# Kernel tuning notes

Hardware: AMD Instinct MI355X
Metric: run time of the kernel (lower is better)

The kernel has to match this reference:

```python
import jax, jax.numpy as jnp
import numpy as np

EPS = 1e-5
GN_GROUPS = 4  # ConvBlock groupnorm num_groups

def _conv3d(x, w, b):
    # x: [B,C,D,H,W], w: [O,I,3,3,3]
    y = jax.lax.conv_general_dilated(x, w, (1, 1, 1), 'SAME',
                                     dimension_numbers=('NCDHW', 'OIDHW', 'NCDHW'))
    return y + b[None, :, None, None, None]

def _groupnorm(x, gamma, beta):
    b, c, d, h, w = x.shape
    xg = x.reshape(b, GN_GROUPS, c // GN_GROUPS, d, h, w)
    m = xg.mean(axis=(2, 3, 4, 5), keepdims=True)
    v = xg.var(axis=(2, 3, 4, 5), keepdims=True)
    xn = ((xg - m) * jax.lax.rsqrt(v + EPS)).reshape(b, c, d, h, w)
    return xn * gamma[None, :, None, None, None] + beta[None, :, None, None, None]

def setup_inputs() -> dict:
    key = jax.random.key(0)
    ks = jax.random.split(key, 8)
    B, C, D, H, W = 4, 64, 16, 16, 16
    R = 4
    f = lambda k, s: jax.random.normal(k, s, dtype=jnp.float32) * 0.05
    return {
        'x': jax.random.normal(ks[0], (B, C, D, H, W), dtype=jnp.float32),
        'w_i': f(ks[1], (C, C, 3, 3, 3)), 'b_i': jnp.zeros((C,), jnp.float32),
        'gamma_i': jnp.ones((C,), jnp.float32), 'beta_i': jnp.zeros((C,), jnp.float32),
        'w_q': f(ks[2], (C // R, C)), 'b_q': jnp.zeros((C // R,), jnp.float32),
        'w_k': f(ks[3], (C // R, C)), 'b_k': jnp.zeros((C // R,), jnp.float32),
        'w_v': f(ks[4], (C, C)), 'b_v': jnp.zeros((C,), jnp.float32),
        'w_o': f(ks[5], (C, C, 3, 3, 3)), 'b_o': jnp.zeros((C,), jnp.float32),
        'gamma_o': jnp.ones((C,), jnp.float32), 'beta_o': jnp.zeros((C,), jnp.float32),
    }

def reference(x, w_i, b_i, gamma_i, beta_i, w_q, b_q, w_k, b_k, w_v, b_v,
              w_o, b_o, gamma_o, beta_o):
    # i_conv: Conv3d(3x3x3) -> GroupNorm(4) -> ReLU
    x = jax.nn.relu(_groupnorm(_conv3d(x, w_i, b_i), gamma_i, beta_i))
    b, c, d, h, w = x.shape
    n = d * h * w
    xf = x.reshape(b, c, n)
    # spatial attention (groups=1): conv1x1 projections as channel matmuls
    q = jnp.einsum('oc,bcn->bon', w_q, xf) + b_q[None, :, None]   # [b, c/r, n]
    k = jnp.einsum('oc,bcn->bon', w_k, xf) + b_k[None, :, None]   # [b, c/r, n]
    v = jnp.einsum('oc,bcn->bon', w_v, xf) + b_v[None, :, None]   # [b, c,   n]
    A = jax.nn.softmax(jnp.einsum('bqn,bqm->bnm', q, k), axis=-1)  # [b, n, n]
    # ans = bmm(value, A^T): ans[b,c,m] = sum_n v[b,c,n] * A[b,m,n]
    sa = jnp.einsum('bcn,bmn->bcm', v, A).reshape(b, c, d, h, w)
    # channel attention
    Ac = jax.nn.softmax(jnp.einsum('bcn,bdn->bcd', xf, xf), axis=-1)  # [b, c, c]
    ca = jnp.einsum('bcd,bdn->bcn', Ac, xf).reshape(b, c, d, h, w)
    y = x + sa + ca
    # o_conv
    return jax.nn.relu(_groupnorm(_conv3d(y, w_o, b_o), gamma_o, beta_o))
```

## Files before the change

### kernel.cpp

```cpp
#include <hip/hip_runtime.h>

#define OFF_T0  0
#define OFF_SA  1048576
#define OFF_QT  2097152
#define OFF_KT  2359296
#define OFF_VB  2621440
#define OFF_YT  3145728
#define OFF_XB  3670016
#define OFF_AC  4194304
#define OFF_WBI 4210688
#define OFF_WBO 4265984
#define OFF_PT  4321280
#define OFF_PO  4325376
#define OFF_MS  6422528
#define WS_NEED ((size_t)6553600 * 4)

typedef __attribute__((ext_vector_type(8))) short short8v;
typedef __attribute__((ext_vector_type(4))) short short4v;
typedef __attribute__((ext_vector_type(4))) float f32x4;

__device__ __forceinline__ ushort f2bf(float f) {
  union { float f; unsigned u; } v; v.f = f;
  unsigned r = (v.u + 0x7fffu + ((v.u >> 16) & 1u)) >> 16;
  return (ushort)r;
}
__device__ __forceinline__ float bf2f(ushort u) {
  union { unsigned u; float f; } v; v.u = ((unsigned)u) << 16;
  return v.f;
}

__global__ __launch_bounds__(256) void wcvt2_k(const float* __restrict__ wi, const float* __restrict__ wo,
    ushort* __restrict__ wbi, ushort* __restrict__ wbo) {
  int idx = blockIdx.x * 256 + threadIdx.x;
  const float* w = idx < 110592 ? wi : wo;
  ushort* wb = idx < 110592 ? wbi : wbo;
  int j = idx < 110592 ? idx : idx - 110592;
  int ci = j & 63, tap = (j >> 6) % 27, co = j / (64 * 27);
  wb[j] = f2bf(w[(co * 64 + ci) * 27 + tap]);
}

__global__ __launch_bounds__(256) void xcvt_k(const float* __restrict__ x, ushort* __restrict__ xb,
    float* __restrict__ pt) {
  if (blockIdx.x == 0 && threadIdx.x < 64) pt[threadIdx.x] = 0.f;
  __shared__ ushort tl[64 * 72];
  int b = blockIdx.x >> 6;
  int n0 = (blockIdx.x & 63) * 64;
  int t = threadIdx.x;
  int ci = t >> 2, q = t & 3;
  const float* src = x + (size_t)(b * 64 + ci) * 4096 + n0 + q * 16;
  #pragma unroll
  for (int i = 0; i < 4; ++i) {
    float4 v = *reinterpret_cast<const float4*>(src + i * 4);
    tl[(q * 16 + i * 4 + 0) * 72 + ci] = f2bf(v.x);
    tl[(q * 16 + i * 4 + 1) * 72 + ci] = f2bf(v.y);
    tl[(q * 16 + i * 4 + 2) * 72 + ci] = f2bf(v.z);
    tl[(q * 16 + i * 4 + 3) * 72 + ci] = f2bf(v.w);
  }
  __syncthreads();
  int n = t >> 2, qq = t & 3;
  ushort* dst = xb + (size_t)(b * 4096 + n0 + n) * 64 + qq * 16;
  *reinterpret_cast<short8v*>(dst) = *reinterpret_cast<const short8v*>(&tl[n * 72 + qq * 16]);
  *reinterpret_cast<short8v*>(dst + 8) = *reinterpret_cast<const short8v*>(&tl[n * 72 + qq * 16 + 8]);
}

__global__ __launch_bounds__(256) void conv_mfma_k(const ushort* __restrict__ xt,
    const ushort* __restrict__ wb, const float* __restrict__ bias, float* __restrict__ out,
    float* __restrict__ ptg) {
  __shared__ __align__(16) ushort xls[18 * 18 * 64];
  __shared__ float sh_st[16];
  int blk = blockIdx.x;
  int h0 = (blk & 3) * 4;
  int d0 = (blk >> 2) & 15;
  int b  = blk >> 6;
  int tid = threadIdx.x;

  const ushort* xtb = xt + (size_t)b * 4096 * 64;
  for (int u = tid; u < 324; u += 256) {
    int w_s = u % 18;
    int row = u / 18;
    int dz = row / 6, h_s = row - dz * 6;
    int d = d0 + dz - 1, h = h0 + h_s - 1, w = w_s - 1;
    ushort* dst = &xls[(row * 18 + w_s) * 64];
    int swz = w_s & 7;
    if (d >= 0 && d < 16 && h >= 0 && h < 16 && w >= 0 && w < 16) {
      const ushort* src = xtb + (size_t)(d * 256 + h * 16 + w) * 64;
      #pragma unroll
      for (int c = 0; c < 8; ++c)
        *reinterpret_cast<short8v*>(dst + ((c ^ swz) << 3)) =
            *reinterpret_cast<const short8v*>(src + (c << 3));
    } else {
      short8v z = {};
      #pragma unroll
      for (int c = 0; c < 8; ++c)
        *reinterpret_cast<short8v*>(dst + ((c ^ swz) << 3)) = z;
    }
  }
  __syncthreads();

  int wv = tid >> 6, l = tid & 63;
  int wn = wv >> 1, wc = wv & 1;
  int lm = l & 15, lg = l >> 4;

  f32x4 acc[2][2] = {};
  const ushort* wbase0 = wb + (size_t)((wc * 2 + 0) * 16 + lm) * 1728 + lg * 8;
  const ushort* wbase1 = wb + (size_t)((wc * 2 + 1) * 16 + lm) * 1728 + lg * 8;

  #pragma unroll 6
  for (int s = 0; s < 54; ++s) {
    int tap = s >> 1, c0h = s & 1;
    int dz = tap / 9, dyx = tap - dz * 9;
    int dy = dyx / 3, dx = dyx - dy * 3;
    int wrow = lm + dx;
    int chunk = ((c0h * 4 + lg) ^ (wrow & 7)) << 3;
    int r0 = ((dz * 6 + wn * 2 + dy) * 18 + wrow) * 64 + chunk;
    short8v a0 = *reinterpret_cast<const short8v*>(&xls[r0]);
    short8v a1 = *reinterpret_cast<const short8v*>(&xls[r0 + 18 * 64]);
    short8v b0 = *reinterpret_cast<const short8v*>(wbase0 + s * 32);
    short8v b1 = *reinterpret_cast<const short8v*>(wbase1 + s * 32);
    acc[0][0] = __builtin_amdgcn_mfma_f32_16x16x32_bf16(a0, b0, acc[0][0], 0, 0, 0);
    acc[0][1] = __builtin_amdgcn_mfma_f32_16x16x32_bf16(a0, b1, acc[0][1], 0, 0, 0);
    acc[1][0] = __builtin_amdgcn_mfma_f32_16x16x32_bf16(a1, b0, acc[1][0], 0, 0, 0);
    acc[1][1] = __builtin_amdgcn_mfma_f32_16x16x32_bf16(a1, b1, acc[1][1], 0, 0, 0);
  }

  float gs[2], gss[2];
  #pragma unroll
  for (int j = 0; j < 2; ++j) {
    gs[j] = 0.f; gss[j] = 0.f;
    int co = (wc * 2 + j) * 16 + lm;
    float bs = bias[co];
    #pragma unroll
    for (int i = 0; i < 2; ++i) {
      int hh = h0 + wn * 2 + i;
      float4 o;
      o.x = acc[i][j][0] + bs; o.y = acc[i][j][1] + bs;
      o.z = acc[i][j][2] + bs; o.w = acc[i][j][3] + bs;
      gs[j]  += o.x + o.y + o.z + o.w;
      gss[j] = fmaf(o.x, o.x, gss[j]); gss[j] = fmaf(o.y, o.y, gss[j]);
      gss[j] = fmaf(o.z, o.z, gss[j]); gss[j] = fmaf(o.w, o.w, gss[j]);
      *reinterpret_cast<float4*>(&out[(size_t)(b * 64 + co) * 4096 + d0 * 256 + hh * 16 + lg * 4]) = o;
    }
  }
  #pragma unroll
  for (int j = 0; j < 2; ++j) {
    #pragma unroll
    for (int off = 32; off > 0; off >>= 1) {
      gs[j]  += __shfl_xor(gs[j], off);
      gss[j] += __shfl_xor(gss[j], off);
    }
    if (l == 0) { sh_st[wv * 4 + j * 2] = gs[j]; sh_st[wv * 4 + j * 2 + 1] = gss[j]; }
  }
  __syncthreads();
  if (tid < 8) {
    int g = tid >> 1, w2 = tid & 1;
    int wcg = g >> 1, j = g & 1;
    float v = sh_st[wcg * 4 + j * 2 + w2] + sh_st[(wcg + 2) * 4 + j * 2 + w2];
    atomicAdd(&ptg[(b * 4 + g) * 2 + w2], v);
  }
}

__global__ __launch_bounds__(256) void gn_apply_k(const float* __restrict__ t, const float* __restrict__ pt,
    const float* __restrict__ gamma, const float* __restrict__ beta, float* __restrict__ out) {
  int idx = blockIdx.x * 256 + threadIdx.x;
  int c = (idx >> 12) & 63, b = idx >> 18;
  int bg = b * 4 + (c >> 4);
  float s0 = pt[bg * 2], ss0 = pt[bg * 2 + 1];
  float m = s0 * (1.f / 65536.f);
  float r = rsqrtf(ss0 * (1.f / 65536.f) - m * m + 1e-5f);
  float ga = r * gamma[c], bb2 = beta[c] - m * r * gamma[c];
  out[idx] = fmaxf(fmaf(t[idx], ga, bb2), 0.f);
}

__global__ __launch_bounds__(256) void proj_all_k(const float* __restrict__ t0, const float* __restrict__ pt0,
    const float* __restrict__ gamma, const float* __restrict__ beta,
    const float* __restrict__ wq, const float* __restrict__ bq,
    const float* __restrict__ wk, const float* __restrict__ bk,
    const float* __restrict__ wv_, const float* __restrict__ bv,
    ushort* __restrict__ qt, ushort* __restrict__ kt, ushort* __restrict__ vt) {
  __shared__ float xls[64 * 68];
  int b = blockIdx.x >> 6, n0 = (blockIdx.x & 63) * 64;
  int tid = threadIdx.x;
  {
    int ci = tid >> 2, q = tid & 3;
    int bg = b * 4 + (ci >> 4);
    float s0 = pt0[bg * 2], ss0 = pt0[bg * 2 + 1];
    float m = s0 * (1.f / 65536.f);
    float rv = rsqrtf(ss0 * (1.f / 65536.f) - m * m + 1e-5f);
    float ga = rv * gamma[ci], bb2 = beta[ci] - m * rv * gamma[ci];
    const float* src = t0 + (size_t)(b * 64 + ci) * 4096 + n0 + q * 16;
    #pragma unroll
    for (int i = 0; i < 4; ++i) {
      float4 v = *reinterpret_cast<const float4*>(src + i * 4);
      float* d = &xls[ci * 68 + q * 16 + i * 4];
      d[0] = fmaxf(fmaf(v.x, ga, bb2), 0.f);
      d[1] = fmaxf(fmaf(v.y, ga, bb2), 0.f);
      d[2] = fmaxf(fmaf(v.z, ga, bb2), 0.f);
      d[3] = fmaxf(fmaf(v.w, ga, bb2), 0.f);
    }
  }
  __syncthreads();
  int n = tid & 63, og = tid >> 6;
  float xr[64];
  #pragma unroll
  for (int c = 0; c < 64; ++c) xr[c] = xls[c * 68 + n];
  if (og < 2) {
    const float* w  = og == 0 ? wq : wk;
    const float* bb = og == 0 ? bq : bk;
    float scale = og == 0 ? 1.4426950408889634f : 1.0f;
    ushort* outp = og == 0 ? qt : kt;
    union { ushort u[16]; short8v v[2]; } pk;
    #pragma unroll
    for (int o = 0; o < 16; ++o) {
      const float* wr = w + o * 64;
      float acc = bb[o];
      #pragma unroll
      for (int c = 0; c < 64; ++c) acc = fmaf(wr[c], xr[c], acc);
      pk.u[o] = f2bf(acc * scale);
    }
    ushort* dst = outp + (size_t)(b * 4096 + n0 + n) * 32;
    *reinterpret_cast<short8v*>(dst) = pk.v[0];
    *reinterpret_cast<short8v*>(dst + 8) = pk.v[1];
    short8v z = {};
    *reinterpret_cast<short8v*>(dst + 16) = z;
    *reinterpret_cast<short8v*>(dst + 24) = z;
  } else {
    int o0 = (og - 2) * 32;
    #pragma unroll
    for (int o = 0; o < 32; ++o) {
      const float* wr = wv_ + (o0 + o) * 64;
      float acc = bv[o0 + o];
      #pragma unroll
      for (int c = 0; c < 64; ++c) acc = fmaf(wr[c], xr[c], acc);
      vt[(size_t)(b * 64 + o0 + o) * 4096 + n0 + n] = f2bf(acc);
    }
  }
}

#define KP 40
#define VP 72
template<bool SPLIT>
__global__ __launch_bounds__(256) void flash_mfma_k(const ushort* __restrict__ qt,
    const ushort* __restrict__ kt, const ushort* __restrict__ vb, float* __restrict__ sa,
    ushort* __restrict__ pacc, float* __restrict__ pms) {
  __shared__ __align__(16) ushort kls[2][64 * KP];
  __shared__ __align__(16) ushort vls[2][64 * VP];
  __shared__ __align__(16) ushort pls[64 * VP];
  int s, mt, b;
  if (SPLIT) { s = blockIdx.x & 3; mt = (blockIdx.x >> 2) & 63; b = blockIdx.x >> 8; }
  else       { s = 0; mt = blockIdx.x & 63; b = blockIdx.x >> 6; }
  const int NT = SPLIT ? 16 : 64;
  int m0 = mt * 64;
  int kofs = s * 1024;
  int tid = threadIdx.x;
  int w = tid >> 6, l = tid & 63;
  int lm = l & 15, lg = l >> 4;

  short8v qf = *reinterpret_cast<const short8v*>(
      qt + (size_t)(b * 4096 + m0 + w * 16 + lm) * 32 + lg * 8);

  f32x4 acc[4] = {};
  float M = -1e30f, S = 0.f;

  int sr = tid >> 2, sq = tid & 3;
  const ushort* ksrc = kt + (size_t)b * 4096 * 32 + (size_t)kofs * 32 + (size_t)sr * 32 + sq * 8;
  const ushort* vsrc = vb + (size_t)b * 64 * 4096 + (size_t)sr * 4096 + kofs + sq * 16;
  int koff = sr * KP + sq * 8;
  int voff = sr * VP + sq * 16;

  {
    short8v kr = *reinterpret_cast<const short8v*>(ksrc);
    short8v v0 = *reinterpret_cast<const short8v*>(vsrc);
    short8v v1 = *reinterpret_cast<const short8v*>(vsrc + 8);
    *reinterpret_cast<short8v*>(&kls[0][koff]) = kr;
    *reinterpret_cast<short8v*>(&vls[0][voff]) = v0;
    *reinterpret_cast<short8v*>(&vls[0][voff + 8]) = v1;
  }

  ushort* plb = &pls[(w * 16 + lm) * VP];

  #pragma unroll 2
  for (int it = 0; it < NT; ++it) {
    int cur = it & 1;
    int nx = it < NT - 1 ? it + 1 : NT - 1;
    short8v knr = *reinterpret_cast<const short8v*>(ksrc + (size_t)nx * 2048);
    short8v vn0 = *reinterpret_cast<const short8v*>(vsrc + nx * 64);
    short8v vn1 = *reinterpret_cast<const short8v*>(vsrc + nx * 64 + 8);

    __syncthreads();

    const ushort* kb  = &kls[cur][0];
    const ushort* vbk = &vls[cur][0];

    f32x4 sf[4];
    #pragma unroll
    for (int nt = 0; nt < 4; ++nt) {
      short8v kf = *reinterpret_cast<const short8v*>(&kb[(nt * 16 + lm) * KP + lg * 8]);
      f32x4 z = {};
      sf[nt] = __builtin_amdgcn_mfma_f32_16x16x32_bf16(kf, qf, z, 0, 0, 0);
    }

    float tmax = -1e30f;
    #pragma unroll
    for (int nt = 0; nt < 4; ++nt)
      #pragma unroll
      for (int r = 0; r < 4; ++r) tmax = fmaxf(tmax, sf[nt][r]);
    tmax = fmaxf(tmax, __shfl_xor(tmax, 16));
    tmax = fmaxf(tmax, __shfl_xor(tmax, 32));
    if (!__all(tmax <= M)) {
      float Mn = fmaxf(M, tmax);
      float sc = __builtin_amdgcn_exp2f(M - Mn);
      M = Mn;
      S *= sc;
      #pragma unroll
      for (int ct = 0; ct < 4; ++ct)
        #pragma unroll
        for (int r = 0; r < 4; ++r) acc[ct][r] *= sc;
    }
    float tsum = 0.f;
    float p[16];
    #pragma unroll
    for (int nt = 0; nt < 4; ++nt)
      #pragma unroll
      for (int r = 0; r < 4; ++r) {
        float e = __builtin_amdgcn_exp2f(sf[nt][r] - M);
        p[nt * 4 + r] = e;
        tsum += e;
      }
    tsum += __shfl_xor(tsum, 16);
    tsum += __shfl_xor(tsum, 32);
    S += tsum;

    #pragma unroll
    for (int nt = 0; nt < 4; ++nt) {
      unsigned p01, p23;
      asm("v_cvt_pk_bf16_f32 %0, %1, %2" : "=v"(p01) : "v"(p[nt * 4 + 0]), "v"(p[nt * 4 + 1]));
      asm("v_cvt_pk_bf16_f32 %0, %1, %2" : "=v"(p23) : "v"(p[nt * 4 + 2]), "v"(p[nt * 4 + 3]));
      union { unsigned u[2]; short4v v; } pk;
      pk.u[0] = p01; pk.u[1] = p23;
      *reinterpret_cast<short4v*>(plb + nt * 16 + lg * 4) = pk.v;
    }
    asm volatile("s_waitcnt lgkmcnt(0)" ::: "memory");
    __builtin_amdgcn_sched_barrier(0);

    #pragma unroll
    for (int nh = 0; nh < 2; ++nh) {
      short8v pf = *reinterpret_cast<const short8v*>(plb + nh * 32 + lg * 8);
      #pragma unroll
      for (int ct = 0; ct < 4; ++ct) {
        short8v vf = *reinterpret_cast<const short8v*>(&vbk[(ct * 16 + lm) * VP + nh * 32 + lg * 8]);
        acc[ct] = __builtin_amdgcn_mfma_f32_16x16x32_bf16(vf, pf, acc[ct], 0, 0, 0);
      }
    }

    if (it < NT - 1) {
      *reinterpret_cast<short8v*>(&kls[cur ^ 1][koff]) = knr;
      *reinterpret_cast<short8v*>(&vls[cur ^ 1][voff]) = vn0;
      *reinterpret_cast<short8v*>(&vls[cur ^ 1][voff + 8]) = vn1;
    }
  }

  if (SPLIT) {
    int blk = (b * 64 + mt) * 4 + s;
    ushort* pa = pacc + (size_t)blk * 4096;
    #pragma unroll
    for (int ct = 0; ct < 4; ++ct)
      #pragma unroll
      for (int r = 0; r < 4; ++r)
        pa[(ct * 16 + lg * 4 + r) * 64 + w * 16 + lm] = f2bf(acc[ct][r]);
    if (l < 16) {
      pms[(size_t)blk * 128 + (w * 16 + lm) * 2]     = M;
      pms[(size_t)blk * 128 + (w * 16 + lm) * 2 + 1] = S;
    }
  } else {
    float inv = 1.f / S;
    #pragma unroll
    for (int ct = 0; ct < 4; ++ct)
      #pragma unroll
      for (int r = 0; r < 4; ++r)
        sa[(size_t)(b * 64 + ct * 16 + lg * 4 + r) * 4096 + m0 + w * 16 + lm] = acc[ct][r] * inv;
  }
}

__global__ __launch_bounds__(256) void gram_partial_k(const float* __restrict__ t0,
    const float* __restrict__ pt0, const float* __restrict__ gamma, const float* __restrict__ beta,
    float* __restrict__ pg) {
  __shared__ __align__(16) ushort hi[64 * 64];
  __shared__ __align__(16) ushort lo[64 * 64];
  int b = blockIdx.x >> 5, ks = blockIdx.x & 31;
  int tid = threadIdx.x;
  int wv = tid >> 6, l = tid & 63, lm = l & 15, lg = l >> 4;
  int wr = wv >> 1, wd = wv & 1;
  f32x4 acc[2][2] = {};
  int sr = tid >> 2, sq = tid & 3;
  int bg = b * 4 + (sr >> 4);
  float s0p = pt0[bg * 2], ss0p = pt0[bg * 2 + 1];
  float mq = s0p * (1.f / 65536.f);
  float rq = rsqrtf(ss0p * (1.f / 65536.f) - mq * mq + 1e-5f);
  float ga = rq * gamma[sr], bb2 = beta[sr] - mq * rq * gamma[sr];
  const float* xb = t0 + (size_t)b * 262144;

  for (int kt = 0; kt < 2; ++kt) {
    int n0 = ks * 128 + kt * 64;
    __syncthreads();
    const float* src = xb + (size_t)sr * 4096 + n0 + sq * 16;
    #pragma unroll
    for (int c2 = 0; c2 < 2; ++c2) {
      int chunk = sq * 2 + c2;
      int dchunk = chunk ^ (sr & 7);
      short8v hvv, lvv;
      #pragma unroll
      for (int j = 0; j < 8; ++j) {
        float v = fmaxf(fmaf(src[c2 * 8 + j], ga, bb2), 0.f);
        ushort hb = f2bf(v);
        union { float f; unsigned u; } uu; uu.u = ((unsigned)hb) << 16;
        hvv[j] = (short)hb;
        lvv[j] = (short)f2bf(v - uu.f);
      }
      *reinterpret_cast<short8v*>(&hi[sr * 64 + dchunk * 8]) = hvv;
      *reinterpret_cast<short8v*>(&lo[sr * 64 + dchunk * 8]) = lvv;
    }
    __syncthreads();
    #pragma unroll
    for (int kk = 0; kk < 2; ++kk) {
      short8v ah[2], al[2], bh[2], bl[2];
      #pragma unroll
      for (int i = 0; i < 2; ++i) {
        int rc = wr * 32 + i * 16 + lm;
        int ca = ((kk * 4 + lg) ^ (rc & 7)) * 8;
        ah[i] = *reinterpret_cast<const short8v*>(&hi[rc * 64 + ca]);
        al[i] = *reinterpret_cast<const short8v*>(&lo[rc * 64 + ca]);
        int rd = wd * 32 + i * 16 + lm;
        int cb = ((kk * 4 + lg) ^ (rd & 7)) * 8;
        bh[i] = *reinterpret_cast<const short8v*>(&hi[rd * 64 + cb]);
        bl[i] = *reinterpret_cast<const short8v*>(&lo[rd * 64 + cb]);
      }
      #pragma unroll
      for (int i = 0; i < 2; ++i)
        #pragma unroll
        for (int j = 0; j < 2; ++j) {
          acc[i][j] = __builtin_amdgcn_mfma_f32_16x16x32_bf16(ah[i], bh[j], acc[i][j], 0, 0, 0);
          acc[i][j] = __builtin_amdgcn_mfma_f32_16x16x32_bf16(ah[i], bl[j], acc[i][j], 0, 0, 0);
          acc[i][j] = __builtin_amdgcn_mfma_f32_16x16x32_bf16(al[i], bh[j], acc[i][j], 0, 0, 0);
        }
    }
  }
  float* pgb = pg + (size_t)blockIdx.x * 4096;
  #pragma unroll
  for (int i = 0; i < 2; ++i)
    #pragma unroll
    for (int j = 0; j < 2; ++j)
      #pragma unroll
      for (int r = 0; r < 4; ++r) {
        int c = wr * 32 + i * 16 + lg * 4 + r;
        int d = wd * 32 + j * 16 + lm;
        pgb[c * 64 + d] = acc[i][j][r];
      }
}

__global__ __launch_bounds__(256) void gram_softmax_k(const float* __restrict__ pg, float* __restrict__ Ac) {
  int b = blockIdx.x;
  int t = threadIdx.x;
  int r = t >> 2, q = t & 3;
  float4 s[4] = {};
  for (int ks = 0; ks < 32; ++ks) {
    const float* row = pg + ((size_t)(b * 32 + ks) * 64 + r) * 64 + q * 16;
    #pragma unroll
    for (int i = 0; i < 4; ++i) {
      float4 v = *reinterpret_cast<const float4*>(row + i * 4);
      s[i].x += v.x; s[i].y += v.y; s[i].z += v.z; s[i].w += v.w;
    }
  }
  float mx = -1e30f;
  #pragma unroll
  for (int i = 0; i < 4; ++i)
    mx = fmaxf(mx, fmaxf(fmaxf(s[i].x, s[i].y), fmaxf(s[i].z, s[i].w)));
  mx = fmaxf(mx, __shfl_xor(mx, 1));
  mx = fmaxf(mx, __shfl_xor(mx, 2));
  float sum = 0.f;
  #pragma unroll
  for (int i = 0; i < 4; ++i) {
    s[i].x = __expf(s[i].x - mx); s[i].y = __expf(s[i].y - mx);
    s[i].z = __expf(s[i].z - mx); s[i].w = __expf(s[i].w - mx);
    sum += s[i].x + s[i].y + s[i].z + s[i].w;
  }
  sum += __shfl_xor(sum, 1);
  sum += __shfl_xor(sum, 2);
  float inv = 1.f / sum;
  float* dst = Ac + ((size_t)(b * 64 + r)) * 64 + q * 16;
  #pragma unroll
  for (int i = 0; i < 4; ++i) {
    float4 o; o.x = s[i].x * inv; o.y = s[i].y * inv; o.z = s[i].z * inv; o.w = s[i].w * inv;
    *reinterpret_cast<float4*>(dst + i * 4) = o;
  }
}

template<int NSPLIT>
__global__ __launch_bounds__(256) void ca_apply_k(const float* __restrict__ t0,
    const float* __restrict__ pt0, const float* __restrict__ gamma, const float* __restrict__ beta,
    const float* __restrict__ Ac, const float* __restrict__ sa,
    const ushort* __restrict__ pacc, const float* __restrict__ pms, ushort* __restrict__ yt) {
  __shared__ float x1f[64 * 72];
  __shared__ float acf[64 * 72];
  __shared__ float wls[4 * 64];
  int b = blockIdx.x >> 6, mt = blockIdx.x & 63;
  int n0 = mt * 64;
  int tid = threadIdx.x;
  {
    int d = tid >> 2, q = tid & 3;
    int bg = b * 4 + (d >> 4);
    float s0p = pt0[bg * 2], ss0p = pt0[bg * 2 + 1];
    float mq = s0p * (1.f / 65536.f);
    float rq = rsqrtf(ss0p * (1.f / 65536.f) - mq * mq + 1e-5f);
    float ga = rq * gamma[d], bb2 = beta[d] - mq * rq * gamma[d];
    const float* xs = t0 + (size_t)(b * 64 + d) * 4096 + n0 + q * 16;
    const float* as = Ac + (size_t)(b * 64 + d) * 64 + q * 16;
    #pragma unroll
    for (int i = 0; i < 4; ++i) {
      float4 v = *reinterpret_cast<const float4*>(xs + i * 4);
      x1f[d * 72 + q * 16 + i * 4 + 0] = fmaxf(fmaf(v.x, ga, bb2), 0.f);
      x1f[d * 72 + q * 16 + i * 4 + 1] = fmaxf(fmaf(v.y, ga, bb2), 0.f);
      x1f[d * 72 + q * 16 + i * 4 + 2] = fmaxf(fmaf(v.z, ga, bb2), 0.f);
      x1f[d * 72 + q * 16 + i * 4 + 3] = fmaxf(fmaf(v.w, ga, bb2), 0.f);
      float4 a = *reinterpret_cast<const float4*>(as + i * 4);
      acf[d * 72 + q * 16 + i * 4 + 0] = a.x;
      acf[d * 72 + q * 16 + i * 4 + 1] = a.y;
      acf[d * 72 + q * 16 + i * 4 + 2] = a.z;
      acf[d * 72 + q * 16 + i * 4 + 3] = a.w;
    }
  }
  if (NSPLIT > 1 && tid < 64) {
    int m = tid;
    size_t msb = (size_t)(b * 64 + mt) * NSPLIT * 128;
    float Ms[NSPLIT], Ss[NSPLIT];
    float Mg = -1e30f;
    #pragma unroll
    for (int s = 0; s < NSPLIT; ++s) {
      Ms[s] = pms[msb + s * 128 + m * 2];
      Ss[s] = pms[msb + s * 128 + m * 2 + 1];
      Mg = fmaxf(Mg, Ms[s]);
    }
    float Stot = 0.f;
    #pragma unroll
    for (int s = 0; s < NSPLIT; ++s) {
      float wv = __builtin_amdgcn_exp2f(Ms[s] - Mg);
      wls[s * 64 + m] = wv;
      Stot += wv * Ss[s];
    }
    float inv = 1.f / Stot;
    #pragma unroll
    for (int s = 0; s < NSPLIT; ++s) wls[s * 64 + m] *= inv;
  }
  __syncthreads();
  int m = tid & 63, cg = tid >> 6;
  float sval[16];
  if (NSPLIT > 1) {
    #pragma unroll
    for (int ci = 0; ci < 16; ++ci) sval[ci] = 0.f;
    const ushort* pb = pacc + (size_t)(b * 64 + mt) * NSPLIT * 4096;
    #pragma unroll
    for (int s = 0; s < NSPLIT; ++s) {
      float wv = wls[s * 64 + m];
      #pragma unroll
      for (int ci = 0; ci < 16; ++ci)
        sval[ci] = fmaf(wv, bf2f(pb[s * 4096 + (cg * 16 + ci) * 64 + m]), sval[ci]);
    }
  } else {
    #pragma unroll
    for (int ci = 0; ci < 16; ++ci)
      sval[ci] = sa[(size_t)(b * 64 + cg * 16 + ci) * 4096 + n0 + m];
  }
  float xcol[64];
  #pragma unroll
  for (int d = 0; d < 64; ++d) xcol[d] = x1f[d * 72 + m];
  union { ushort u[16]; short8v v[2]; } pk;
  #pragma unroll
  for (int ci = 0; ci < 16; ++ci) {
    int c = cg * 16 + ci;
    float o = xcol[c] + sval[ci];
    const float* ar = &acf[c * 72];
    #pragma unroll
    for (int d4 = 0; d4 < 16; ++d4) {
      float4 a4 = *reinterpret_cast<const float4*>(ar + d4 * 4);
      o = fmaf(a4.x, xcol[d4 * 4 + 0], o);
      o = fmaf(a4.y, xcol[d4 * 4 + 1], o);
      o = fmaf(a4.z, xcol[d4 * 4 + 2], o);
      o = fmaf(a4.w, xcol[d4 * 4 + 3], o);
    }
    pk.u[ci] = f2bf(o);
  }
  ushort* dst = yt + (size_t)(b * 4096 + n0 + m) * 64 + cg * 16;
  *reinterpret_cast<short8v*>(dst) = pk.v[0];
  *reinterpret_cast<short8v*>(dst + 8) = pk.v[1];
}

extern "C" void kernel_launch(void* const* d_in, const int* in_sizes, int n_in,
                              void* d_out, int out_size, void* d_ws, size_t ws_size,
                              hipStream_t stream) {
  const float* x       = (const float*)d_in[0];
  const float* w_i     = (const float*)d_in[1];
  const float* b_i     = (const float*)d_in[2];
  const float* gamma_i = (const float*)d_in[3];
  const float* beta_i  = (const float*)d_in[4];
  const float* w_q     = (const float*)d_in[5];
  const float* b_q     = (const float*)d_in[6];
  const float* w_k     = (const float*)d_in[7];
  const float* b_k     = (const float*)d_in[8];
  const float* w_v     = (const float*)d_in[9];
  const float* b_v     = (const float*)d_in[10];
  const float* w_o     = (const float*)d_in[11];
  const float* b_o     = (const float*)d_in[12];
  const float* gamma_o = (const float*)d_in[13];
  const float* beta_o  = (const float*)d_in[14];
  float* ws = (float*)d_ws;
  float* t0 = ws + OFF_T0;
  ushort* qt  = (ushort*)(ws + OFF_QT);
  ushort* kt  = (ushort*)(ws + OFF_KT);
  ushort* vbp = (ushort*)(ws + OFF_VB);
  float* yb = ws + OFF_SA;
  float* pg = ws + OFF_QT;
  ushort* ytp = (ushort*)(ws + OFF_YT);
  ushort* xbp = (ushort*)(ws + OFF_XB);
  float* ac = ws + OFF_AC;
  ushort* wbi = (ushort*)(ws + OFF_WBI);
  ushort* wbo = (ushort*)(ws + OFF_WBO);
  float* pt0 = ws + OFF_PT;
  float* pt1 = pt0 + 32;
  ushort* pacc = (ushort*)(ws + OFF_PO);
  float* pms  = ws + OFF_MS;
  float* outp = (float*)d_out;
  bool split = ws_size >= WS_NEED;

  wcvt2_k<<<864, 256, 0, stream>>>(w_i, w_o, wbi, wbo);
  xcvt_k<<<256, 256, 0, stream>>>(x, xbp, pt0);

  conv_mfma_k<<<256, 256, 0, stream>>>(xbp, wbi, b_i, t0, pt0);

  proj_all_k<<<256, 256, 0, stream>>>(t0, pt0, gamma_i, beta_i,
                                      w_q, b_q, w_k, b_k, w_v, b_v, qt, kt, vbp);

  if (split)
    flash_mfma_k<true><<<1024, 256, 0, stream>>>(qt, kt, vbp, yb, pacc, pms);
  else
    flash_mfma_k<false><<<256, 256, 0, stream>>>(qt, kt, vbp, yb, pacc, pms);

  gram_partial_k<<<128, 256, 0, stream>>>(t0, pt0, gamma_i, beta_i, pg);
  gram_softmax_k<<<4, 256, 0, stream>>>(pg, ac);

  if (split)
    ca_apply_k<4><<<256, 256, 0, stream>>>(t0, pt0, gamma_i, beta_i, ac, yb, pacc, pms, ytp);
  else
    ca_apply_k<1><<<256, 256, 0, stream>>>(t0, pt0, gamma_i, beta_i, ac, yb, pacc, pms, ytp);

  conv_mfma_k<<<256, 256, 0, stream>>>(ytp, wbo, b_o, t0, pt1);
  gn_apply_k<<<4096, 256, 0, stream>>>(t0, pt1, gamma_o, beta_o, outp);
}
```

Before: 138.4 us.

## Merge small kernels and double block counts for conv, projection and CA stages

Fuses the weight and input bf16 conversion kernels into one launch, and fuses the flash-attention split and Gram partial kernels into one heterogeneous launch that shares shared memory. Doubles the grid for conv, projection and channel-attention apply by halving per-block channel or row work, so more of the GPU's compute units are occupied. Also uses a max3 tree for the row max in flash attention. Costs include redundant halo loads in conv (each block now loads the full tile for half the output channels) and the Gram partial buffer moving to the SA region.

After: 151.5 us. 1.1x slower.

```diff
diff --git a/kernel.cpp b/kernel.cpp
--- a/kernel.cpp
+++ b/kernel.cpp
@@ -28,39 +28,43 @@
   union { unsigned u; float f; } v; v.u = ((unsigned)u) << 16;
   return v.f;
 }
-
-__global__ __launch_bounds__(256) void wcvt2_k(const float* __restrict__ wi, const float* __restrict__ wo,
+__device__ __forceinline__ float max3f(float a, float b, float c) {
+  return fmaxf(fmaxf(a, b), c);
+}
+
+__global__ __launch_bounds__(256) void cvt_k(const float* __restrict__ x, ushort* __restrict__ xb,
+    float* __restrict__ pt, const float* __restrict__ wi, const float* __restrict__ wo,
     ushort* __restrict__ wbi, ushort* __restrict__ wbo) {
-  int idx = blockIdx.x * 256 + threadIdx.x;
-  const float* w = idx < 110592 ? wi : wo;
-  ushort* wb = idx < 110592 ? wbi : wbo;
-  int j = idx < 110592 ? idx : idx - 110592;
-  int ci = j & 63, tap = (j >> 6) % 27, co = j / (64 * 27);
-  wb[j] = f2bf(w[(co * 64 + ci) * 27 + tap]);
-}
-
-__global__ __launch_bounds__(256) void xcvt_k(const float* __restrict__ x, ushort* __restrict__ xb,
-    float* __restrict__ pt) {
-  if (blockIdx.x == 0 && threadIdx.x < 64) pt[threadIdx.x] = 0.f;
   __shared__ ushort tl[64 * 72];
-  int b = blockIdx.x >> 6;
-  int n0 = (blockIdx.x & 63) * 64;
+  int blk = blockIdx.x;
   int t = threadIdx.x;
-  int ci = t >> 2, q = t & 3;
-  const float* src = x + (size_t)(b * 64 + ci) * 4096 + n0 + q * 16;
-  #pragma unroll
-  for (int i = 0; i < 4; ++i) {
-    float4 v = *reinterpret_cast<const float4*>(src + i * 4);
-    tl[(q * 16 + i * 4 + 0) * 72 + ci] = f2bf(v.x);
-    tl[(q * 16 + i * 4 + 1) * 72 + ci] = f2bf(v.y);
-    tl[(q * 16 + i * 4 + 2) * 72 + ci] = f2bf(v.z);
-    tl[(q * 16 + i * 4 + 3) * 72 + ci] = f2bf(v.w);
-  }
-  __syncthreads();
-  int n = t >> 2, qq = t & 3;
-  ushort* dst = xb + (size_t)(b * 4096 + n0 + n) * 64 + qq * 16;
-  *reinterpret_cast<short8v*>(dst) = *reinterpret_cast<const short8v*>(&tl[n * 72 + qq * 16]);
-  *reinterpret_cast<short8v*>(dst + 8) = *reinterpret_cast<const short8v*>(&tl[n * 72 + qq * 16 + 8]);
+  if (blk < 256) {
+    if (blk == 0 && t < 64) pt[t] = 0.f;
+    int b = blk >> 6;
+    int n0 = (blk & 63) * 64;
+    int ci = t >> 2, q = t & 3;
+    const float* src = x + (size_t)(b * 64 + ci) * 4096 + n0 + q * 16;
+    #pragma unroll
+    for (int i = 0; i < 4; ++i) {
+      float4 v = *reinterpret_cast<const float4*>(src + i * 4);
+      tl[(q * 16 + i * 4 + 0) * 72 + ci] = f2bf(v.x);
+      tl[(q * 16 + i * 4 + 1) * 72 + ci] = f2bf(v.y);
+      tl[(q * 16 + i * 4 + 2) * 72 + ci] = f2bf(v.z);
+      tl[(q * 16 + i * 4 + 3) * 72 + ci] = f2bf(v.w);
+    }
+    __syncthreads();
+    int n = t >> 2, qq = t & 3;
+    ushort* dst = xb + (size_t)(b * 4096 + n0 + n) * 64 + qq * 16;
+    *reinterpret_cast<short8v*>(dst) = *reinterpret_cast<const short8v*>(&tl[n * 72 + qq * 16]);
+    *reinterpret_cast<short8v*>(dst + 8) = *reinterpret_cast<const short8v*>(&tl[n * 72 + qq * 16 + 8]);
+  } else {
+    int idx = (blk - 256) * 256 + t;
+    const float* w = idx < 110592 ? wi : wo;
+    ushort* wb = idx < 110592 ? wbi : wbo;
+    int j = idx < 110592 ? idx : idx - 110592;
+    int ci = j & 63, tap = (j >> 6) % 27, co = j / (64 * 27);
+    wb[j] = f2bf(w[(co * 64 + ci) * 27 + tap]);
+  }
 }
 
 __global__ __launch_bounds__(256) void conv_mfma_k(const ushort* __restrict__ xt,
@@ -69,9 +73,10 @@
   __shared__ __align__(16) ushort xls[18 * 18 * 64];
   __shared__ float sh_st[16];
   int blk = blockIdx.x;
-  int h0 = (blk & 3) * 4;
-  int d0 = (blk >> 2) & 15;
-  int b  = blk >> 6;
+  int s2 = blk & 1;
+  int h0 = ((blk >> 1) & 3) * 4;
+  int d0 = (blk >> 3) & 15;
+  int b  = blk >> 7;
   int tid = threadIdx.x;
 
   const ushort* xtb = xt + (size_t)b * 4096 * 64;
@@ -97,13 +102,12 @@
   }
   __syncthreads();
 
-  int wv = tid >> 6, l = tid & 63;
-  int wn = wv >> 1, wc = wv & 1;
-  int lm = l & 15, lg = l >> 4;
-
-  f32x4 acc[2][2] = {};
-  const ushort* wbase0 = wb + (size_t)((wc * 2 + 0) * 16 + lm) * 1728 + lg * 8;
-  const ushort* wbase1 = wb + (size_t)((wc * 2 + 1) * 16 + lm) * 1728 + lg * 8;
+  int wn = tid >> 6;
+  int l = tid & 63, lm = l & 15, lg = l >> 4;
+
+  f32x4 acc[2] = {};
+  const ushort* wbase0 = wb + (size_t)((s2 * 2 + 0) * 16 + lm) * 1728 + lg * 8;
+  const ushort* wbase1 = wb + (size_t)((s2 * 2 + 1) * 16 + lm) * 1728 + lg * 8;
 
   #pragma unroll 6
   for (int s = 0; s < 54; ++s) {
@@ -112,34 +116,28 @@
     int dy = dyx / 3, dx = dyx - dy * 3;
     int wrow = lm + dx;
     int chunk = ((c0h * 4 + lg) ^ (wrow & 7)) << 3;
-    int r0 = ((dz * 6 + wn * 2 + dy) * 18 + wrow) * 64 + chunk;
+    int r0 = ((dz * 6 + wn + dy) * 18 + wrow) * 64 + chunk;
     short8v a0 = *reinterpret_cast<const short8v*>(&xls[r0]);
-    short8v a1 = *reinterpret_cast<const short8v*>(&xls[r0 + 18 * 64]);
     short8v b0 = *reinterpret_cast<const short8v*>(wbase0 + s * 32);
     short8v b1 = *reinterpret_cast<const short8v*>(wbase1 + s * 32);
-    acc[0][0] = __builtin_amdgcn_mfma_f32_16x16x32_bf16(a0, b0, acc[0][0], 0, 0, 0);
-    acc[0][1] = __builtin_amdgcn_mfma_f32_16x16x32_bf16(a0, b1, acc[0][1], 0, 0, 0);
-    acc[1][0] = __builtin_amdgcn_mfma_f32_16x16x32_bf16(a1, b0, acc[1][0], 0, 0, 0);
-    acc[1][1] = __builtin_amdgcn_mfma_f32_16x16x32_bf16(a1, b1, acc[1][1], 0, 0, 0);
+    acc[0] = __builtin_amdgcn_mfma_f32_16x16x32_bf16(a0, b0, acc[0], 0, 0, 0);
+    acc[1] = __builtin_amdgcn_mfma_f32_16x16x32_bf16(a0, b1, acc[1], 0, 0, 0);
   }
 
   float gs[2], gss[2];
+  int hh = h0 + wn;
   #pragma unroll
   for (int j = 0; j < 2; ++j) {
     gs[j] = 0.f; gss[j] = 0.f;
-    int co = (wc * 2 + j) * 16 + lm;
+    int co = (s2 * 2 + j) * 16 + lm;
     float bs = bias[co];
-    #pragma unroll
-    for (int i = 0; i < 2; ++i) {
-      int hh = h0 + wn * 2 + i;
-      float4 o;
-      o.x = acc[i][j][0] + bs; o.y = acc[i][j][1] + bs;
-      o.z = acc[i][j][2] + bs; o.w = acc[i][j][3] + bs;
-      gs[j]  += o.x + o.y + o.z + o.w;
-      gss[j] = fmaf(o.x, o.x, gss[j]); gss[j] = fmaf(o.y, o.y, gss[j]);
-      gss[j] = fmaf(o.z, o.z, gss[j]); gss[j] = fmaf(o.w, o.w, gss[j]);
-      *reinterpret_cast<float4*>(&out[(size_t)(b * 64 + co) * 4096 + d0 * 256 + hh * 16 + lg * 4]) = o;
-    }
+    float4 o;
+    o.x = acc[j][0] + bs; o.y = acc[j][1] + bs;
+    o.z = acc[j][2] + bs; o.w = acc[j][3] + bs;
+    gs[j]  = o.x + o.y + o.z + o.w;
+    gss[j] = fmaf(o.x, o.x, gss[j]); gss[j] = fmaf(o.y, o.y, gss[j]);
+    gss[j] = fmaf(o.z, o.z, gss[j]); gss[j] = fmaf(o.w, o.w, gss[j]);
+    *reinterpret_cast<float4*>(&out[(size_t)(b * 64 + co) * 4096 + d0 * 256 + hh * 16 + lg * 4]) = o;
   }
   #pragma unroll
   for (int j = 0; j < 2; ++j) {
@@ -148,14 +146,14 @@
       gs[j]  += __shfl_xor(gs[j], off);
       gss[j] += __shfl_xor(gss[j], off);
     }
-    if (l == 0) { sh_st[wv * 4 + j * 2] = gs[j]; sh_st[wv * 4 + j * 2 + 1] = gss[j]; }
+    if (l == 0) { sh_st[wn * 4 + j * 2] = gs[j]; sh_st[wn * 4 + j * 2 + 1] = gss[j]; }
   }
   __syncthreads();
-  if (tid < 8) {
-    int g = tid >> 1, w2 = tid & 1;
-    int wcg = g >> 1, j = g & 1;
-    float v = sh_st[wcg * 4 + j * 2 + w2] + sh_st[(wcg + 2) * 4 + j * 2 + w2];
-    atomicAdd(&ptg[(b * 4 + g) * 2 + w2], v);
+  if (tid < 4) {
+    int j = tid >> 1, w2 = tid & 1;
+    float v = sh_st[0 * 4 + j * 2 + w2] + sh_st[1 * 4 + j * 2 + w2] +
+              sh_st[2 * 4 + j * 2 + w2] + sh_st[3 * 4 + j * 2 + w2];
+    atomicAdd(&ptg[(b * 4 + s2 * 2 + j) * 2 + w2], v);
   }
 }
 
@@ -178,7 +176,10 @@
     const float* __restrict__ wv_, const float* __restrict__ bv,
     ushort* __restrict__ qt, ushort* __restrict__ kt, ushort* __restrict__ vt) {
   __shared__ float xls[64 * 68];
-  int b = blockIdx.x >> 6, n0 = (blockIdx.x & 63) * 64;
+  int blk = blockIdx.x;
+  int half = blk & 1;
+  int n0 = ((blk >> 1) & 63) * 64;
+  int b = blk >> 7;
   int tid = threadIdx.x;
   {
     int ci = tid >> 2, q = tid & 3;
@@ -203,30 +204,29 @@
   float xr[64];
   #pragma unroll
   for (int c = 0; c < 64; ++c) xr[c] = xls[c * 68 + n];
-  if (og < 2) {
-    const float* w  = og == 0 ? wq : wk;
-    const float* bb = og == 0 ? bq : bk;
-    float scale = og == 0 ? 1.4426950408889634f : 1.0f;
-    ushort* outp = og == 0 ? qt : kt;
-    union { ushort u[16]; short8v v[2]; } pk;
-    #pragma unroll
-    for (int o = 0; o < 16; ++o) {
-      const float* wr = w + o * 64;
-      float acc = bb[o];
+  if (half == 0) {
+    const float* w  = og < 2 ? wq : wk;
+    const float* bb = og < 2 ? bq : bk;
+    float scale = og < 2 ? 1.4426950408889634f : 1.0f;
+    ushort* outp = og < 2 ? qt : kt;
+    int o0 = (og & 1) * 8;
+    union { ushort u[8]; short8v v; } pk;
+    #pragma unroll
+    for (int o = 0; o < 8; ++o) {
+      const float* wr = w + (o0 + o) * 64;
+      float acc = bb[o0 + o];
       #pragma unroll
       for (int c = 0; c < 64; ++c) acc = fmaf(wr[c], xr[c], acc);
       pk.u[o] = f2bf(acc * scale);
     }
     ushort* dst = outp + (size_t)(b * 4096 + n0 + n) * 32;
-    *reinterpret_cast<short8v*>(dst) = pk.v[0];
-    *reinterpret_cast<short8v*>(dst + 8) = pk.v[1];
+    *reinterpret_cast<short8v*>(dst + o0) = pk.v;
     short8v z = {};
-    *reinterpret_cast<short8v*>(dst + 16) = z;
-    *reinterpret_cast<short8v*>(dst + 24) = z;
+    *reinterpret_cast<short8v*>(dst + 16 + o0) = z;
   } else {
-    int o0 = (og - 2) * 32;
-    #pragma unroll
-    for (int o = 0; o < 32; ++o) {
+    int o0 = og * 16;
+    #pragma unroll
+    for (int o = 0; o < 16; ++o) {
       const float* wr = wv_ + (o0 + o) * 64;
       float acc = bv[o0 + o];
       #pragma unroll
@@ -239,15 +239,15 @@
 #define KP 40
 #define VP 72
 template<bool SPLIT>
-__global__ __launch_bounds__(256) void flash_mfma_k(const ushort* __restrict__ qt,
+__device__ __forceinline__ void flash_body(const ushort* __restrict__ qt,
     const ushort* __restrict__ kt, const ushort* __restrict__ vb, float* __restrict__ sa,
-    ushort* __restrict__ pacc, float* __restrict__ pms) {
-  __shared__ __align__(16) ushort kls[2][64 * KP];
-  __shared__ __align__(16) ushort vls[2][64 * VP];
-  __shared__ __align__(16) ushort pls[64 * VP];
+    ushort* __restrict__ pacc, float* __restrict__ pms, ushort* smem, int fblk) {
+  ushort* kls = smem;
+  ushort* vls = smem + 5120;
+  ushort* pls = smem + 14336;
   int s, mt, b;
-  if (SPLIT) { s = blockIdx.x & 3; mt = (blockIdx.x >> 2) & 63; b = blockIdx.x >> 8; }
-  else       { s = 0; mt = blockIdx.x & 63; b = blockIdx.x >> 6; }
+  if (SPLIT) { s = fblk & 3; mt = (fblk >> 2) & 63; b = fblk >> 8; }
+  else       { s = 0; mt = fblk & 63; b = fblk >> 6; }
   const int NT = SPLIT ? 16 : 64;
   int m0 = mt * 64;
   int kofs = s * 1024;
@@ -271,12 +271,12 @@
     short8v kr = *reinterpret_cast<const short8v*>(ksrc);
     short8v v0 = *reinterpret_cast<const short8v*>(vsrc);
     short8v v1 = *reinterpret_cast<const short8v*>(vsrc + 8);
-    *reinterpret_cast<short8v*>(&kls[0][koff]) = kr;
-    *reinterpret_cast<short8v*>(&vls[0][voff]) = v0;
-    *reinterpret_cast<short8v*>(&vls[0][voff + 8]) = v1;
-  }
-
-  ushort* plb = &pls[(w * 16 + lm) * VP];
+    *reinterpret_cast<short8v*>(kls + koff) = kr;
+    *reinterpret_cast<short8v*>(vls + voff) = v0;
+    *reinterpret_cast<short8v*>(vls + voff + 8) = v1;
+  }
+
+  ushort* plb = pls + (w * 16 + lm) * VP;
 
   #pragma unroll 2
   for (int it = 0; it < NT; ++it) {
@@ -288,8 +288,8 @@
 
     __syncthreads();
 
-    const ushort* kb  = &kls[cur][0];
-    const ushort* vbk = &vls[cur][0];
+    const ushort* kb  = kls + cur * 2560;
+    const ushort* vbk = vls + cur * 4608;
 
     f32x4 sf[4];
     #pragma unroll
@@ -299,11 +299,12 @@
       sf[nt] = __builtin_amdgcn_mfma_f32_16x16x32_bf16(kf, qf, z, 0, 0, 0);
     }
 
-    float tmax = -1e30f;
-    #pragma unroll
-    for (int nt = 0; nt < 4; ++nt)
-      #pragma unroll
-      for (int r = 0; r < 4; ++r) tmax = fmaxf(tmax, sf[nt][r]);
+    float t0_ = max3f(sf[0][0], sf[0][1], sf[0][2]);
+    float t1_ = max3f(sf[0][3], sf[1][0], sf[1][1]);
+    float t2_ = max3f(sf[1][2], sf[1][3], sf[2][0]);
+    float t3_ = max3f(sf[2][1], sf[2][2], sf[2][3]);
+    float t4_ = max3f(sf[3][0], sf[3][1], sf[3][2]);
+    float tmax = fmaxf(max3f(t0_, t1_, t2_), max3f(t3_, t4_, sf[3][3]));
     tmax = fmaxf(tmax, __shfl_xor(tmax, 16));
     tmax = fmaxf(tmax, __shfl_xor(tmax, 32));
     if (!__all(tmax <= M)) {
@@ -353,23 +354,23 @@
     }
 
     if (it < NT - 1) {
-      *reinterpret_cast<short8v*>(&kls[cur ^ 1][koff]) = knr;
-      *reinterpret_cast<short8v*>(&vls[cur ^ 1][voff]) = vn0;
-      *reinterpret_cast<short8v*>(&vls[cur ^ 1][voff + 8]) = vn1;
+      *reinterpret_cast<short8v*>(kls + (cur ^ 1) * 2560 + koff) = knr;
+      *reinterpret_cast<short8v*>(vls + (cur ^ 1) * 4608 + voff) = vn0;
+      *reinterpret_cast<short8v*>(vls + (cur ^ 1) * 4608 + voff + 8) = vn1;
     }
   }
 
   if (SPLIT) {
-    int blk = (b * 64 + mt) * 4 + s;
-    ushort* pa = pacc + (size_t)blk * 4096;
+    int blk2 = (b * 64 + mt) * 4 + s;
+    ushort* pa = pacc + (size_t)blk2 * 4096;
     #pragma unroll
     for (int ct = 0; ct < 4; ++ct)
       #pragma unroll
       for (int r = 0; r < 4; ++r)
         pa[(ct * 16 + lg * 4 + r) * 64 + w * 16 + lm] = f2bf(acc[ct][r]);
     if (l < 16) {
-      pms[(size_t)blk * 128 + (w * 16 + lm) * 2]     = M;
-      pms[(size_t)blk * 128 + (w * 16 + lm) * 2 + 1] = S;
+      pms[(size_t)blk2 * 128 + (w * 16 + lm) * 2]     = M;
+      pms[(size_t)blk2 * 128 + (w * 16 + lm) * 2 + 1] = S;
     }
   } else {
     float inv = 1.f / S;
@@ -381,12 +382,10 @@
   }
 }
 
-__global__ __launch_bounds__(256) void gram_partial_k(const float* __restrict__ t0,
+__device__ __forceinline__ void gram_body(const float* __restrict__ t0,
     const float* __restrict__ pt0, const float* __restrict__ gamma, const float* __restrict__ beta,
-    float* __restrict__ pg) {
-  __shared__ __align__(16) ushort hi[64 * 64];
-  __shared__ __align__(16) ushort lo[64 * 64];
-  int b = blockIdx.x >> 5, ks = blockIdx.x & 31;
+    float* __restrict__ pg, ushort* hi, ushort* lo, int gblk) {
+  int b = gblk >> 5, ks = gblk & 31;
   int tid = threadIdx.x;
   int wv = tid >> 6, l = tid & 63, lm = l & 15, lg = l >> 4;
   int wr = wv >> 1, wd = wv & 1;
@@ -416,8 +415,8 @@
         hvv[j] = (short)hb;
         lvv[j] = (short)f2bf(v - uu.f);
       }
-      *reinterpret_cast<short8v*>(&hi[sr * 64 + dchunk * 8]) = hvv;
-      *reinterpret_cast<short8v*>(&lo[sr * 64 + dchunk * 8]) = lvv;
+      *reinterpret_cast<short8v*>(hi + sr * 64 + dchunk * 8) = hvv;
+      *reinterpret_cast<short8v*>(lo + sr * 64 + dchunk * 8) = lvv;
     }
     __syncthreads();
     #pragma unroll
@@ -427,12 +426,12 @@
       for (int i = 0; i < 2; ++i) {
         int rc = wr * 32 + i * 16 + lm;
         int ca = ((kk * 4 + lg) ^ (rc & 7)) * 8;
-        ah[i] = *reinterpret_cast<const short8v*>(&hi[rc * 64 + ca]);
-        al[i] = *reinterpret_cast<const short8v*>(&lo[rc * 64 + ca]);
+        ah[i] = *reinterpret_cast<const short8v*>(hi + rc * 64 + ca);
+        al[i] = *reinterpret_cast<const short8v*>(lo + rc * 64 + ca);
         int rd = wd * 32 + i * 16 + lm;
         int cb = ((kk * 4 + lg) ^ (rd & 7)) * 8;
-        bh[i] = *reinterpret_cast<const short8v*>(&hi[rd * 64 + cb]);
-        bl[i] = *reinterpret_cast<const short8v*>(&lo[rd * 64 + cb]);
+        bh[i] = *reinterpret_cast<const short8v*>(hi + rd * 64 + cb);
+        bl[i] = *reinterpret_cast<const short8v*>(lo + rd * 64 + cb);
       }
       #pragma unroll
       for (int i = 0; i < 2; ++i)
@@ -444,7 +443,7 @@
         }
     }
   }
-  float* pgb = pg + (size_t)blockIdx.x * 4096;
+  float* pgb = pg + (size_t)gblk * 4096;
   #pragma unroll
   for (int i = 0; i < 2; ++i)
     #pragma unroll
@@ -455,6 +454,32 @@
         int d = wd * 32 + j * 16 + lm;
         pgb[c * 64 + d] = acc[i][j][r];
       }
+}
+
+__global__ __launch_bounds__(256) void flash_gram_k(const ushort* __restrict__ qt,
+    const ushort* __restrict__ kt, const ushort* __restrict__ vb,
+    ushort* __restrict__ pacc, float* __restrict__ pms,
+    const float* __restrict__ t0, const float* __restrict__ pt0,
+    const float* __restrict__ gamma, const float* __restrict__ beta, float* __restrict__ pg) {
+  __shared__ __align__(16) ushort smem[18944];
+  int blk = blockIdx.x;
+  if (blk < 128) {
+    gram_body(t0, pt0, gamma, beta, pg, smem, smem + 4096, blk);
+  } else {
+    flash_body<true>(qt, kt, vb, nullptr, pacc, pms, smem, blk - 128);
+  }
+}
+
+__global__ __launch_bounds__(256) void flash_fb_k(const ushort* __restrict__ qt,
+    const ushort* __restrict__ kt, const ushort* __restrict__ vb, float* __restrict__ sa) {
+  __shared__ __align__(16) ushort smem[18944];
+  flash_body<false>(qt, kt, vb, sa, nullptr, nullptr, smem, blockIdx.x);
+}
+__global__ __launch_bounds__(256) void gram_fb_k(const float* __restrict__ t0,
+    const float* __restrict__ pt0, const float* __restrict__ gamma, const float* __restrict__ beta,
+    float* __restrict__ pg) {
+  __shared__ __align__(16) ushort smem[8192];
+  gram_body(t0, pt0, gamma, beta, pg, smem, smem + 4096, blockIdx.x);
 }
 
 __global__ __launch_bounds__(256) void gram_softmax_k(const float* __restrict__ pg, float* __restrict__ Ac) {
@@ -502,7 +527,10 @@
   __shared__ float x1f[64 * 72];
   __shared__ float acf[64 * 72];
   __shared__ float wls[4 * 64];
-  int b = blockIdx.x >> 6, mt = blockIdx.x & 63;
+  int blk = blockIdx.x;
+  int chalf = blk & 1;
+  int mt = (blk >> 1) & 63;
+  int b = blk >> 7;
   int n0 = mt * 64;
   int tid = threadIdx.x;
   {
@@ -551,31 +579,31 @@
     for (int s = 0; s < NSPLIT; ++s) wls[s * 64 + m] *= inv;
   }
   __syncthreads();
-  int m = tid & 63, cg = tid >> 6;
-  float sval[16];
+  int m = tid & 63, cg8 = chalf * 4 + (tid >> 6);
+  float sval[8];
   if (NSPLIT > 1) {
     #pragma unroll
-    for (int ci = 0; ci < 16; ++ci) sval[ci] = 0.f;
+    for (int ci = 0; ci < 8; ++ci) sval[ci] = 0.f;
     const ushort* pb = pacc + (size_t)(b * 64 + mt) * NSPLIT * 4096;
     #pragma unroll
     for (int s = 0; s < NSPLIT; ++s) {
       float wv = wls[s * 64 + m];
       #pragma unroll
-      for (int ci = 0; ci < 16; ++ci)
-        sval[ci] = fmaf(wv, bf2f(pb[s * 4096 + (cg * 16 + ci) * 64 + m]), sval[ci]);
+      for (int ci = 0; ci < 8; ++ci)
+        sval[ci] = fmaf(wv, bf2f(pb[s * 4096 + (cg8 * 8 + ci) * 64 + m]), sval[ci]);
     }
   } else {
     #pragma unroll
-    for (int ci = 0; ci < 16; ++ci)
-      sval[ci] = sa[(size_t)(b * 64 + cg * 16 + ci) * 4096 + n0 + m];
+    for (int ci = 0; ci < 8; ++ci)
+      sval[ci] = sa[(size_t)(b * 64 + cg8 * 8 + ci) * 4096 + n0 + m];
   }
   float xcol[64];
   #pragma unroll
   for (int d = 0; d < 64; ++d) xcol[d] = x1f[d * 72 + m];
-  union { ushort u[16]; short8v v[2]; } pk;
-  #pragma unroll
-  for (int ci = 0; ci < 16; ++ci) {
-    int c = cg * 16 + ci;
+  union { ushort u[8]; short8v v; } pk;
+  #pragma unroll
+  for (int ci = 0; ci < 8; ++ci) {
+    int c = cg8 * 8 + ci;
     float o = xcol[c] + sval[ci];
     const float* ar = &acf[c * 72];
     #pragma unroll
@@ -588,9 +616,8 @@
     }
     pk.u[ci] = f2bf(o);
   }
-  ushort* dst = yt + (size_t)(b * 4096 + n0 + m) * 64 + cg * 16;
-  *reinterpret_cast<short8v*>(dst) = pk.v[0];
-  *reinterpret_cast<short8v*>(dst + 8) = pk.v[1];
+  ushort* dst = yt + (size_t)(b * 4096 + n0 + m) * 64 + cg8 * 8;
+  *reinterpret_cast<short8v*>(dst) = pk.v;
 }
 
 extern "C" void kernel_launch(void* const* d_in, const int* in_sizes, int n_in,
@@ -617,7 +644,6 @@
   ushort* kt  = (ushort*)(ws + OFF_KT);
   ushort* vbp = (ushort*)(ws + OFF_VB);
   float* yb = ws + OFF_SA;
-  float* pg = ws + OFF_QT;
   ushort* ytp = (ushort*)(ws + OFF_YT);
   ushort* xbp = (ushort*)(ws + OFF_XB);
   float* ac = ws + OFF_AC;
@@ -629,28 +655,30 @@
   float* pms  = ws + OFF_MS;
   float* outp = (float*)d_out;
   bool split = ws_size >= WS_NEED;
-
-  wcvt2_k<<<864, 256, 0, stream>>>(w_i, w_o, wbi, wbo);
-  xcvt_k<<<256, 256, 0, stream>>>(x, xbp, pt0);
-
-  conv_mfma_k<<<256, 256, 0, stream>>>(xbp, wbi, b_i, t0, pt0);
-
-  proj_all_k<<<256, 256, 0, stream>>>(t0, pt0, gamma_i, beta_i,
+  float* pg = split ? (ws + OFF_SA) : (ws + OFF_QT);
+
+  cvt_k<<<1120, 256, 0, stream>>>(x, xbp, pt0, w_i, w_o, wbi, wbo);
+
+  conv_mfma_k<<<512, 256, 0, stream>>>(xbp, wbi, b_i, t0, pt0);
+
+  proj_all_k<<<512, 256, 0, stream>>>(t0, pt0, gamma_i, beta_i,
                                       w_q, b_q, w_k, b_k, w_v, b_v, qt, kt, vbp);
 
+  if (split) {
+    flash_gram_k<<<1152, 256, 0, stream>>>(qt, kt, vbp, pacc, pms,
+                                           t0, pt0, gamma_i, beta_i, pg);
+  } else {
+    flash_fb_k<<<256, 256, 0, stream>>>(qt, kt, vbp, yb);
+    gram_fb_k<<<128, 256, 0, stream>>>(t0, pt0, gamma_i, beta_i, pg);
+  }
+
+  gram_softmax_k<<<4, 256, 0, stream>>>(pg, ac);
+
   if (split)
-    flash_mfma_k<true><<<1024, 256, 0, stream>>>(qt, kt, vbp, yb, pacc, pms);
+    ca_apply_k<4><<<512, 256, 0, stream>>>(t0, pt0, gamma_i, beta_i, ac, yb, pacc, pms, ytp);
   else
-    flash_mfma_k<false><<<256, 256, 0, stream>>>(qt, kt, vbp, yb, pacc, pms);
-
-  gram_partial_k<<<128, 256, 0, stream>>>(t0, pt0, gamma_i, beta_i, pg);
-  gram_softmax_k<<<4, 256, 0, stream>>>(pg, ac);
-
-  if (split)
-    ca_apply_k<4><<<256, 256, 0, stream>>>(t0, pt0, gamma_i, beta_i, ac, yb, pacc, pms, ytp);
-  else
-    ca_apply_k<1><<<256, 256, 0, stream>>>(t0, pt0, gamma_i, beta_i, ac, yb, pacc, pms, ytp);
-
-  conv_mfma_k<<<256, 256, 0, stream>>>(ytp, wbo, b_o, t0, pt1);
+    ca_apply_k<1><<<512, 256, 0, stream>>>(t0, pt0, gamma_i, beta_i, ac, yb, pacc, pms, ytp);
+
+  conv_mfma_k<<<512, 256, 0, stream>>>(ytp, wbo, b_o, t0, pt1);
   gn_apply_k<<<4096, 256, 0, stream>>>(t0, pt1, gamma_o, beta_o, outp);
 }
```
